# Kernel tuning notes

Hardware: AMD Instinct MI355X
Metric: run time of the kernel (lower is better)

## Reference

```python
import jax, jax.numpy as jnp
import numpy as np

NUM_HEADS = 16
WINDOW = 128


def apply_rope(x):
    # x: (B, H, S, Dh), standard RoPE with half-split rotation, base 10000
    S, Dh = x.shape[-2], x.shape[-1]
    half = Dh // 2
    inv_freq = 1.0 / (10000.0 ** (jnp.arange(half, dtype=jnp.float32) / half))
    ang = jnp.arange(S, dtype=jnp.float32)[:, None] * inv_freq[None, :]  # (S, half)
    cos, sin = jnp.cos(ang), jnp.sin(ang)
    x1, x2 = x[..., :half], x[..., half:]
    return jnp.concatenate([x1 * cos - x2 * sin, x1 * sin + x2 * cos], axis=-1).astype(x.dtype)


def setup_inputs() -> dict:
    key = jax.random.key(0)
    ks = jax.random.split(key, 5)
    D = 1024
    B, S = 2, 2048
    w = 0.02
    return {
        "x": jax.random.normal(ks[0], (B, S, D), dtype=jnp.float32),
        "Wq": jax.random.normal(ks[1], (D, D), dtype=jnp.float32) * w,
        "bq": jnp.zeros((D,), dtype=jnp.float32),
        "Wk": jax.random.normal(ks[2], (D, D), dtype=jnp.float32) * w,
        "bk": jnp.zeros((D,), dtype=jnp.float32),
        "Wv": jax.random.normal(ks[3], (D, D), dtype=jnp.float32) * w,
        "bv": jnp.zeros((D,), dtype=jnp.float32),
        "Wo": jax.random.normal(ks[4], (D, D), dtype=jnp.float32) * w,
        "bo": jnp.zeros((D,), dtype=jnp.float32),
    }


def reference(x, Wq, bq, Wk, bk, Wv, bv, Wo, bo):
    B, S, D = x.shape
    H = NUM_HEADS
    Dh = D // H

    def proj(W, b):
        y = jnp.einsum("bsd,ed->bse", x, W) + b  # nn.Linear: x @ W.T + b
        return y.reshape(B, S, H, Dh).transpose(0, 2, 1, 3)  # (B,H,S,Dh)

    q = apply_rope(proj(Wq, bq)) * (Dh ** -0.5)
    k = apply_rope(proj(Wk, bk))
    v = proj(Wv, bv)

    scores = jnp.einsum("bhqd,bhkd->bhqk", q, k)  # (B,H,S,S)
    idx = jnp.arange(S)
    rel = idx[None, :] - idx[:, None]  # k - q
    blocked = (rel > 0) | (rel < -WINDOW)  # True = masked out
    scores = jnp.where(blocked[None, None], -jnp.inf, scores)
    probs = jax.nn.softmax(scores, axis=-1)
    out = jnp.einsum("bhqk,bhkd->bhqd", probs, v)
    out = out.transpose(0, 2, 1, 3).reshape(B, S, D)
    return jnp.einsum("bsd,ed->bse", out, Wo) + bo
```

## Files before the change

kernel.cpp:

```cpp
#include <hip/hip_runtime.h>

typedef __attribute__((ext_vector_type(8)))  short  short8v;
typedef __attribute__((ext_vector_type(8)))  __bf16 bf16x8;
typedef __attribute__((ext_vector_type(4)))  float  f32x4;

__device__ __forceinline__ short f2bf(float f) {
    unsigned u = __builtin_bit_cast(unsigned, f);
    unsigned r = (u + 0x7fffu + ((u >> 16) & 1u)) >> 16;
    return (short)r;
}
__device__ __forceinline__ float lo16(unsigned u) { return __builtin_bit_cast(float, u << 16); }
__device__ __forceinline__ float hi16(unsigned u) { return __builtin_bit_cast(float, u & 0xffff0000u); }

__device__ __forceinline__ void gload16(const void* g, void* l) {
    __builtin_amdgcn_global_load_lds(
        (const __attribute__((address_space(1))) unsigned*)g,
        (__attribute__((address_space(3))) unsigned*)l, 16, 0, 0);
}

__device__ __forceinline__ void ropePair(const uint4& a, const uint4& b,
                                         const float2* cs8, float scale,
                                         uint4& oa, uint4& ob) {
    const unsigned au[4] = {a.x, a.y, a.z, a.w}, bu[4] = {b.x, b.y, b.z, b.w};
    unsigned ra[4], rb[4];
    #pragma unroll
    for (int wi = 0; wi < 4; ++wi) {
        const float x1l = lo16(au[wi]), x1h = hi16(au[wi]);
        const float x2l = lo16(bu[wi]), x2h = hi16(bu[wi]);
        const float2 cl = cs8[wi * 2], ch = cs8[wi * 2 + 1];
        const float o1l = (x1l * cl.x - x2l * cl.y) * scale;
        const float o2l = (x1l * cl.y + x2l * cl.x) * scale;
        const float o1h = (x1h * ch.x - x2h * ch.y) * scale;
        const float o2h = (x1h * ch.y + x2h * ch.x) * scale;
        ra[wi] = (unsigned)(unsigned short)f2bf(o1l) | ((unsigned)(unsigned short)f2bf(o1h) << 16);
        rb[wi] = (unsigned)(unsigned short)f2bf(o2l) | ((unsigned)(unsigned short)f2bf(o2h) << 16);
    }
    oa = make_uint4(ra[0], ra[1], ra[2], ra[3]);
    ob = make_uint4(rb[0], rb[1], rb[2], rb[3]);
}

#define S_LEN   2048
#define MAT_ELEMS 4194304

__global__ __launch_bounds__(256) void prep(
    const float* __restrict__ x,  const float* __restrict__ Wq,
    const float* __restrict__ Wk, const float* __restrict__ Wv,
    const float* __restrict__ Wo, const float* __restrict__ bq,
    const float* __restrict__ bk, const float* __restrict__ bv,
    short* __restrict__ xb, short* __restrict__ wcat, short* __restrict__ wob,
    float* __restrict__ bcat, float2* __restrict__ tab)
{
    const int tid = blockIdx.x * 256 + threadIdx.x;
    const float4* src;
    short* dst;
    if (tid < 1048576) {
        src = (const float4*)x + tid;  dst = xb + (size_t)tid * 4;
    } else if (tid < 1835008) {
        const int o = tid - 1048576;
        const int mat = o >> 18;
        const int wi  = o & 262143;
        const float* W = (mat == 0) ? Wq : (mat == 1) ? Wk : Wv;
        src = (const float4*)W + wi;  dst = wcat + (size_t)o * 4;
    } else {
        const int o = tid - 1835008;
        src = (const float4*)Wo + o;  dst = wob + (size_t)o * 4;
    }
    const float4 v = *src;
    short4 s4 = make_short4(f2bf(v.x), f2bf(v.y), f2bf(v.z), f2bf(v.w));
    *(short4*)dst = s4;

    if (tid < 65536) {
        const int s  = tid >> 5;
        const int jr = tid & 31;
        const float freq = exp2f(-(float)jr * (13.287712379549449f / 32.0f));
        const float ang  = (float)s * freq;
        tab[tid] = make_float2(cosf(ang), sinf(ang));
    }
    if (tid < 768) {
        const float* B = (tid < 256) ? bq : (tid < 512) ? bk : bv;
        ((float4*)bcat)[tid] = ((const float4*)B)[tid & 255];
    }
}

#define VMC4 do { asm volatile("s_waitcnt vmcnt(4)" ::: "memory"); __builtin_amdgcn_sched_barrier(0); } while (0)
#define VMC0 do { asm volatile("s_waitcnt vmcnt(0)" ::: "memory"); __builtin_amdgcn_sched_barrier(0); } while (0)
#define BAR  __builtin_amdgcn_s_barrier()

#define LOADA(T, PM)                                                      \
  _Pragma("unroll") for (int ii = 0; ii < 4; ++ii) {                      \
    af[ii][0] = ldf(T, fA0, (ii * 32 + (PM) * 128) * 128);                \
    af[ii][1] = ldf(T, fA1, (ii * 32 + (PM) * 128) * 128);                \
  }

#define LOADB(T, PN, BQ)                                                  \
  _Pragma("unroll") for (int jj = 0; jj < 2; ++jj) {                      \
    BQ[jj][0] = ldf(T, fB0, (jj * 64 + (PN) * 128) * 128);                \
    BQ[jj][1] = ldf(T, fB1, (jj * 64 + (PN) * 128) * 128);                \
  }

#define MFMAQ(PM, PN, BQ)                                                     \
  __builtin_amdgcn_s_setprio(1);                                              \
  _Pragma("unroll") for (int ii = 0; ii < 4; ++ii)                            \
    _Pragma("unroll") for (int jj = 0; jj < 2; ++jj) {                        \
      acc[(PM)*4+ii][(PN)*2+jj] = __builtin_amdgcn_mfma_f32_16x16x32_bf16(    \
          af[ii][0], BQ[jj][0], acc[(PM)*4+ii][(PN)*2+jj], 0, 0, 0);          \
      acc[(PM)*4+ii][(PN)*2+jj] = __builtin_amdgcn_mfma_f32_16x16x32_bf16(    \
          af[ii][1], BQ[jj][1], acc[(PM)*4+ii][(PN)*2+jj], 0, 0, 0);          \
    }                                                                         \
  __builtin_amdgcn_s_setprio(0);

#define KTILE(AC, BC, S1, S2, S3, S4, W4)                                 \
  LOADA(AC, 0); LOADB(BC, 0, bq0); S1; BAR; MFMAQ(0, 0, bq0); BAR;        \
  LOADB(BC, 1, bq1); S2; BAR; MFMAQ(0, 1, bq1); BAR;                      \
  LOADA(AC, 1); S3; BAR; MFMAQ(1, 0, bq0); BAR;                           \
  S4; BAR; MFMAQ(1, 1, bq1); W4; BAR;

#define STG(G, KT, H, TILE)                                               \
  { gload16(G + (H) * 262144 + 0     + (KT) * 128, TILE + ((H)*128 + w*16    ) * 64); \
    gload16(G + (H) * 262144 + 16384 + (KT) * 128, TILE + ((H)*128 + w*16 + 8) * 64); }

__global__ __launch_bounds__(512) void gemm8(
    const short* __restrict__ A,
    const short* __restrict__ Bw,
    const float* __restrict__ bias,
    short* __restrict__ outb)
{
    __shared__ short lds[65536];
    short* const Ab0 = lds;
    short* const Bb0 = lds + 16384;
    short* const Ab1 = lds + 32768;
    short* const Bb1 = lds + 49152;

    const int tid = threadIdx.x;
    const int w = tid >> 6, lane = tid & 63;
    const int wm = w >> 2, wn = w & 3;
    const int lr = lane & 15, lg = lane >> 4;

    const int wg  = blockIdx.x;
    const int swz = (wg & 7) * 24 + (wg >> 3);
    const int bx = swz % 12, by = swz / 12;
    const int row0 = by * 256, col0 = bx * 256;

    const int scl  = ((lane & 7) * 16) ^ (((lane >> 3) & 7) << 4);
    const int goff = (w * 16 + (lane >> 3)) * 2048 + scl;
    const char* gA = (const char*)A  + (size_t)row0 * 2048 + goff;
    const char* gB = (const char*)Bw + (size_t)col0 * 2048 + goff;
    const int cswz0 = (lg * 16)      ^ ((lr & 7) << 4);
    const int cswz1 = (64 + lg * 16) ^ ((lr & 7) << 4);
    const int fA0 = (wm * 16 + lr) * 128 + cswz0;
    const int fA1 = (wm * 16 + lr) * 128 + cswz1;
    const int fB0 = (wn * 16 + lr) * 128 + cswz0;
    const int fB1 = (wn * 16 + lr) * 128 + cswz1;

    auto ldf = [&](const short* buf, int voff, int imm) -> bf16x8 {
        return *(const bf16x8*)((const char*)buf + voff + imm);
    };

    f32x4 acc[8][4] = {};
    bf16x8 af[4][2], bq0[2][2], bq1[2][2];

    STG(gA, 0, 0, Ab0);  STG(gB, 0, 0, Bb0);
    STG(gA, 0, 1, Ab0);  STG(gB, 0, 1, Bb0);
    STG(gA, 1, 0, Ab1);  STG(gB, 1, 0, Bb1);
    VMC4;
    BAR;

    #pragma unroll 1
    for (int it = 0; it < 7; ++it) {
        const int t0 = it * 2;
        KTILE(Ab0, Bb0,
              STG(gA, t0 + 1, 1, Ab1),
              STG(gB, t0 + 1, 1, Bb1),
              STG(gA, t0 + 2, 0, Ab0),
              STG(gB, t0 + 2, 0, Bb0), VMC4);
        const int t1 = t0 + 1;
        KTILE(Ab1, Bb1,
              STG(gA, t1 + 1, 1, Ab0),
              STG(gB, t1 + 1, 1, Bb0),
              STG(gA, t1 + 2, 0, Ab1),
              STG(gB, t1 + 2, 0, Bb1), VMC4);
    }
    KTILE(Ab0, Bb0,
          STG(gA, 15, 1, Ab1),
          STG(gB, 15, 1, Bb1), {}, {}, VMC0);
    KTILE(Ab1, Bb1, {}, {}, {}, {}, {});

    const int mat = col0 >> 10;
    const int cm0 = col0 & 1023;
    short* outm = outb + (size_t)mat * MAT_ELEMS;
    #pragma unroll
    for (int j = 0; j < 4; ++j) {
        const int co = wn * 16 + (j & 1) * 64 + (j >> 1) * 128 + lr;
        const float bb = bias[col0 + co];
        #pragma unroll
        for (int i = 0; i < 8; ++i) {
            const int rg = row0 + wm * 16 + (i & 3) * 32 + (i >> 2) * 128 + lg * 4;
            #pragma unroll
            for (int r = 0; r < 4; ++r)
                outm[(size_t)(rg + r) * 1024 + cm0 + co] = f2bf(acc[i][j][r] + bb);
        }
    }
}

__global__ __launch_bounds__(256) void gemm_out(
    const short* __restrict__ A, const short* __restrict__ Bw,
    const float* __restrict__ bias, float* __restrict__ outf)
{
    __shared__ short As[128 * 64];
    __shared__ short Bs[128 * 64];
    const int tid  = threadIdx.x;
    const int w    = tid >> 6, lane = tid & 63;
    const int row0 = blockIdx.y * 128, col0 = blockIdx.x * 128;
    const int wr   = w >> 1, wc = w & 1;
    const int lr   = lane & 15, lg = lane >> 4;
    const int srow = lane >> 3, scol = (lane & 7) * 8;

    f32x4 acc[4][4] = {};

    for (int kt = 0; kt < 16; ++kt) {
        const int k0 = kt * 64;
        __syncthreads();
        #pragma unroll
        for (int rr = 0; rr < 4; ++rr) {
            const int ch = w * 4 + rr;
            const int r  = ch * 8 + srow;
            gload16(A  + (size_t)(row0 + r) * 1024 + k0 + scol, (short*)As + ch * 512);
            gload16(Bw + (size_t)(col0 + r) * 1024 + k0 + scol, (short*)Bs + ch * 512);
        }
        __syncthreads();
        #pragma unroll
        for (int kk = 0; kk < 2; ++kk) {
            const int kb = kk * 32 + lg * 8;
            bf16x8 af[4], bf[4];
            #pragma unroll
            for (int i = 0; i < 4; ++i) {
                af[i] = *(const bf16x8*)&As[(wr * 64 + i * 16 + lr) * 64 + kb];
                bf[i] = *(const bf16x8*)&Bs[(wc * 64 + i * 16 + lr) * 64 + kb];
            }
            #pragma unroll
            for (int i = 0; i < 4; ++i)
                #pragma unroll
                for (int j = 0; j < 4; ++j)
                    acc[i][j] = __builtin_amdgcn_mfma_f32_16x16x32_bf16(af[i], bf[j], acc[i][j], 0, 0, 0);
        }
    }

    #pragma unroll
    for (int i = 0; i < 4; ++i) {
        const int grb = row0 + wr * 64 + i * 16 + lg * 4;
        #pragma unroll
        for (int j = 0; j < 4; ++j) {
            const int cm = col0 + wc * 64 + j * 16 + lr;
            const float bb = bias[cm];
            #pragma unroll
            for (int r = 0; r < 4; ++r)
                outf[(size_t)(grb + r) * 1024 + cm] = acc[i][j][r] + bb;
        }
    }
}

#define KS_ST 72
#define VT_ST 264
#define P_ST  168
__global__ __launch_bounds__(256) void attn_mfma(const short* __restrict__ qkv,
                                                 short* __restrict__ ctx,
                                                 const float2* __restrict__ tab)
{
    __shared__ short lds[27776];
    short* Ks = lds;
    short* VT = lds;
    short* Pl = lds + 16896;
    float* linv = (float*)(lds + 27648);

    const int tid = threadIdx.x;
    const int w = tid >> 6, lane = tid & 63;
    const int g = lane >> 4, l15 = lane & 15;
    const int bid = blockIdx.x;
    const int b  = bid >> 9;
    const int h  = (bid >> 5) & 15;
    const int qb = bid & 31;
    const int qs = qb << 6;
    const size_t rowbase = (size_t)b * S_LEN;
    const int hc = h << 6;

    uint4 vreg[6];
    #pragma unroll
    for (int t = 0; t < 6; ++t) {
        const int c = t * 256 + tid;
        const int key = c >> 3, d0 = c & 7;
        const int gk  = qs - 128 + key;
        const int gkc = gk < 0 ? 0 : gk;
        vreg[t] = *(const uint4*)&qkv[(size_t)2 * MAT_ELEMS + (rowbase + gkc) * 1024 + hc + d0 * 8];
    }

    #pragma unroll
    for (int it = 0; it < 3; ++it) {
        const int c   = it * 256 + tid;
        const int key = c >> 2;
        const int jb  = (c & 3) << 3;
        const int gk  = qs - 128 + key;
        const int gkc = gk < 0 ? 0 : gk;
        const short* kb = qkv + (size_t)1 * MAT_ELEMS + (rowbase + gkc) * 1024 + hc;
        const uint4 k1 = *(const uint4*)(kb + jb);
        const uint4 k2 = *(const uint4*)(kb + jb + 32);
        uint4 o1, o2;
        ropePair(k1, k2, tab + (size_t)gkc * 32 + jb, 1.0f, o1, o2);
        if (gk < 0) { o1 = make_uint4(0, 0, 0, 0); o2 = make_uint4(0, 0, 0, 0); }
        *(uint4*)&Ks[key * KS_ST + jb]      = o1;
        *(uint4*)&Ks[key * KS_ST + jb + 32] = o2;
    }
    __syncthreads();

    const int q = qs + 16 * w + l15;
    const size_t qoff = (rowbase + q) * 1024 + hc;
    const uint4 q1 = *(const uint4*)&qkv[qoff + g * 8];
    const uint4 q2 = *(const uint4*)&qkv[qoff + 32 + g * 8];
    uint4 r1, r2;
    ropePair(q1, q2, tab + (size_t)q * 32 + g * 8, 0.125f, r1, r2);
    const bf16x8 qf0 = __builtin_bit_cast(bf16x8, r1);
    const bf16x8 qf1 = __builtin_bit_cast(bf16x8, r2);

    f32x4 st[9];
    #pragma unroll
    for (int t = 0; t < 9; ++t) {
        const int krow = 16 * w + 16 * t + l15;
        bf16x8 kf0 = *(const bf16x8*)&Ks[krow * KS_ST + g * 8];
        bf16x8 kf1 = *(const bf16x8*)&Ks[krow * KS_ST + 32 + g * 8];
        f32x4 a = {0.f, 0.f, 0.f, 0.f};
        a = __builtin_amdgcn_mfma_f32_16x16x32_bf16(qf0, kf0, a, 0, 0, 0);
        a = __builtin_amdgcn_mfma_f32_16x16x32_bf16(qf1, kf1, a, 0, 0, 0);
        st[t] = a;
    }
    __syncthreads();

    #pragma unroll
    for (int t = 0; t < 6; ++t) {
        const int c = t * 256 + tid;
        const int key = c >> 3, d0 = c & 7;
        const int gk  = qs - 128 + key;
        uint4 vd = vreg[t];
        if (gk < 0) vd = make_uint4(0, 0, 0, 0);
        const unsigned wv[4] = {vd.x, vd.y, vd.z, vd.w};
        #pragma unroll
        for (int e = 0; e < 8; ++e) {
            const short val = (short)(wv[e >> 1] >> (16 * (e & 1)));
            VT[(d0 * 8 + e) * VT_ST + (key ^ (e << 4))] = val;
        }
    }
    {
        const int d  = tid >> 2;
        const int k4 = 12 + (tid & 3);
        const int col0 = (k4 ^ (d & 7)) << 4;
        *(uint4*)&VT[d * VT_ST + col0]     = make_uint4(0, 0, 0, 0);
        *(uint4*)&VT[d * VT_ST + col0 + 8] = make_uint4(0, 0, 0, 0);
    }

    const int jmin = 128 - qs - 16 * w;
    float mrow[4], lsum[4];
    #pragma unroll
    for (int r = 0; r < 4; ++r) mrow[r] = -3.0e38f;
    #pragma unroll
    for (int t = 0; t < 9; ++t) {
        const int jj = 16 * t + l15;
        #pragma unroll
        for (int r = 0; r < 4; ++r) {
            const int qi = 4 * g + r;
            const bool ok = (jj >= qi) && (jj <= qi + 128) && (jj >= jmin);
            if (ok) mrow[r] = fmaxf(mrow[r], st[t][r]);
        }
    }
    #pragma unroll
    for (int r = 0; r < 4; ++r) {
        mrow[r] = fmaxf(mrow[r], __shfl_xor(mrow[r], 1));
        mrow[r] = fmaxf(mrow[r], __shfl_xor(mrow[r], 2));
        mrow[r] = fmaxf(mrow[r], __shfl_xor(mrow[r], 4));
        mrow[r] = fmaxf(mrow[r], __shfl_xor(mrow[r], 8));
        lsum[r] = 0.0f;
    }
    short* Pw = Pl + w * (16 * P_ST);
    #pragma unroll
    for (int t = 0; t < 9; ++t) {
        const int jj = 16 * t + l15;
        #pragma unroll
        for (int r = 0; r < 4; ++r) {
            const int qi = 4 * g + r;
            const bool ok = (jj >= qi) && (jj <= qi + 128) && (jj >= jmin);
            const float p = ok ? __expf(st[t][r] - mrow[r]) : 0.0f;
            lsum[r] += p;
            Pw[qi * P_ST + jj] = f2bf(p);
        }
    }
    {
        short4 z = make_short4(0, 0, 0, 0);
        *(short4*)&Pw[l15 * P_ST + 144 + 4 * g] = z;
    }
    #pragma unroll
    for (int r = 0; r < 4; ++r) {
        lsum[r] += __shfl_xor(lsum[r], 1);
        lsum[r] += __shfl_xor(lsum[r], 2);
        lsum[r] += __shfl_xor(lsum[r], 4);
        lsum[r] += __shfl_xor(lsum[r], 8);
        if (l15 == r) linv[w * 16 + 4 * g + r] = 1.0f / lsum[r];
    }
    __syncthreads();

    f32x4 oc[4] = {};
    #pragma unroll
    for (int kc = 0; kc < 5; ++kc) {
        bf16x8 pf = *(const bf16x8*)&Pw[l15 * P_ST + kc * 32 + g * 8];
        #pragma unroll
        for (int dt = 0; dt < 4; ++dt) {
            const int colb = (16 * w + kc * 32 + g * 8) ^ ((l15 & 7) << 4);
            bf16x8 vf = *(const bf16x8*)&VT[(dt * 16 + l15) * VT_ST + colb];
            oc[dt] = __builtin_amdgcn_mfma_f32_16x16x32_bf16(vf, pf, oc[dt], 0, 0, 0);
        }
    }

    const float inv = linv[w * 16 + l15];
    #pragma unroll
    for (int dt = 0; dt < 4; ++dt) {
        short4 sv;
        sv.x = f2bf(oc[dt][0] * inv);
        sv.y = f2bf(oc[dt][1] * inv);
        sv.z = f2bf(oc[dt][2] * inv);
        sv.w = f2bf(oc[dt][3] * inv);
        *(short4*)&ctx[(rowbase + qs + 16 * w + l15) * 1024 + hc + dt * 16 + 4 * g] = sv;
    }
}

extern "C" void kernel_launch(void* const* d_in, const int* in_sizes, int n_in,
                              void* d_out, int out_size, void* d_ws, size_t ws_size,
                              hipStream_t stream) {
    const float* x  = (const float*)d_in[0];
    const float* Wq = (const float*)d_in[1];
    const float* bq = (const float*)d_in[2];
    const float* Wk = (const float*)d_in[3];
    const float* bk = (const float*)d_in[4];
    const float* Wv = (const float*)d_in[5];
    const float* bv = (const float*)d_in[6];
    const float* Wo = (const float*)d_in[7];
    const float* bo = (const float*)d_in[8];

    char* ws = (char*)d_ws;
    short*  xb   = (short*) (ws + 0);
    short*  wcat = (short*) (ws + 8388608);
    short*  wob  = (short*) (ws + 14680064);
    short*  qkv  = (short*) (ws + 16777216);
    short*  ctx  = (short*) (ws + 41943040);
    float2* tab  = (float2*)(ws + 50331648);
    float*  bcat = (float*) (ws + 50855936);

    prep<<<8192, 256, 0, stream>>>(x, Wq, Wk, Wv, Wo, bq, bk, bv,
                                   xb, wcat, wob, bcat, tab);
    gemm8<<<192, 512, 0, stream>>>(xb, wcat, bcat, qkv);
    attn_mfma<<<1024, 256, 0, stream>>>(qkv, ctx, tab);
    gemm_out<<<dim3(8, 32), 256, 0, stream>>>(ctx, wob, bo, (float*)d_out);
}
```

Before: 95.70 us.

## Restructure GEMM pipeline with double-buffered register fragments and full-tile prefetch

Reworks the QKV GEMM main loop so that A and B register fragments are double-buffered. The next tile's first fragments are loaded from LDS during the current tile's last MFMA quarters, and whole next k-tiles are staged into LDS with a vmcnt(8) wait instead of vmcnt(4). The aim is to hide LDS read latency and global load latency behind MFMA work. Separately, the attention kernel's V-transpose LDS stride is padded from 264 to 266 to reduce bank conflicts, which slightly grows the shared memory footprint. The deeper prefetch raises register and vmcnt pressure and makes the waits harder to get right.

Result: slower. 101.9 us (+6.5%).

```diff
diff --git a/kernel.cpp b/kernel.cpp
--- a/kernel.cpp
+++ b/kernel.cpp
@@ -82,42 +82,44 @@
     }
 }
 
+#define VMC8 do { asm volatile("s_waitcnt vmcnt(8)" ::: "memory"); __builtin_amdgcn_sched_barrier(0); } while (0)
 #define VMC4 do { asm volatile("s_waitcnt vmcnt(4)" ::: "memory"); __builtin_amdgcn_sched_barrier(0); } while (0)
 #define VMC0 do { asm volatile("s_waitcnt vmcnt(0)" ::: "memory"); __builtin_amdgcn_sched_barrier(0); } while (0)
 #define BAR  __builtin_amdgcn_s_barrier()
 
-#define LOADA(T, PM)                                                      \
-  _Pragma("unroll") for (int ii = 0; ii < 4; ++ii) {                      \
-    af[ii][0] = ldf(T, fA0, (ii * 32 + (PM) * 128) * 128);                \
-    af[ii][1] = ldf(T, fA1, (ii * 32 + (PM) * 128) * 128);                \
-  }
-
-#define LOADB(T, PN, BQ)                                                  \
-  _Pragma("unroll") for (int jj = 0; jj < 2; ++jj) {                      \
-    BQ[jj][0] = ldf(T, fB0, (jj * 64 + (PN) * 128) * 128);                \
-    BQ[jj][1] = ldf(T, fB1, (jj * 64 + (PN) * 128) * 128);                \
-  }
-
-#define MFMAQ(PM, PN, BQ)                                                     \
+#define LD_A0(T) _Pragma("unroll") for (int ii = 0; ii < 4; ++ii) { \
+    aA[ii][0] = ldf(T, fA0, (ii * 32) * 128);                        \
+    aA[ii][1] = ldf(T, fA1, (ii * 32) * 128); }
+#define LD_A1(T) _Pragma("unroll") for (int ii = 0; ii < 4; ++ii) { \
+    aB[ii][0] = ldf(T, fA0, (ii * 32 + 128) * 128);                  \
+    aB[ii][1] = ldf(T, fA1, (ii * 32 + 128) * 128); }
+#define LD_B0(T) _Pragma("unroll") for (int jj = 0; jj < 2; ++jj) { \
+    bA[jj][0] = ldf(T, fB0, (jj * 64) * 128);                        \
+    bA[jj][1] = ldf(T, fB1, (jj * 64) * 128); }
+#define LD_B1(T) _Pragma("unroll") for (int jj = 0; jj < 2; ++jj) { \
+    bB[jj][0] = ldf(T, fB0, (jj * 64 + 128) * 128);                  \
+    bB[jj][1] = ldf(T, fB1, (jj * 64 + 128) * 128); }
+
+#define MFQ(PM, PN, AF, BF)                                                   \
   __builtin_amdgcn_s_setprio(1);                                              \
   _Pragma("unroll") for (int ii = 0; ii < 4; ++ii)                            \
     _Pragma("unroll") for (int jj = 0; jj < 2; ++jj) {                        \
       acc[(PM)*4+ii][(PN)*2+jj] = __builtin_amdgcn_mfma_f32_16x16x32_bf16(    \
-          af[ii][0], BQ[jj][0], acc[(PM)*4+ii][(PN)*2+jj], 0, 0, 0);          \
+          AF[ii][0], BF[jj][0], acc[(PM)*4+ii][(PN)*2+jj], 0, 0, 0);          \
       acc[(PM)*4+ii][(PN)*2+jj] = __builtin_amdgcn_mfma_f32_16x16x32_bf16(    \
-          af[ii][1], BQ[jj][1], acc[(PM)*4+ii][(PN)*2+jj], 0, 0, 0);          \
+          AF[ii][1], BF[jj][1], acc[(PM)*4+ii][(PN)*2+jj], 0, 0, 0);          \
     }                                                                         \
   __builtin_amdgcn_s_setprio(0);
 
-#define KTILE(AC, BC, S1, S2, S3, S4, W4)                                 \
-  LOADA(AC, 0); LOADB(BC, 0, bq0); S1; BAR; MFMAQ(0, 0, bq0); BAR;        \
-  LOADB(BC, 1, bq1); S2; BAR; MFMAQ(0, 1, bq1); BAR;                      \
-  LOADA(AC, 1); S3; BAR; MFMAQ(1, 0, bq0); BAR;                           \
-  S4; BAR; MFMAQ(1, 1, bq1); W4; BAR;
-
-#define STG(G, KT, H, TILE)                                               \
-  { gload16(G + (H) * 262144 + 0     + (KT) * 128, TILE + ((H)*128 + w*16    ) * 64); \
-    gload16(G + (H) * 262144 + 16384 + (KT) * 128, TILE + ((H)*128 + w*16 + 8) * 64); }
+#define KT(AC, BC, AN, BN, S1, S2, S3, S4, V1, V2, V3, V4)  \
+  LD_B1(BC); S1; V1; BAR; MFQ(0, 0, aA, bA); BAR;           \
+  LD_A1(AC); S2; V2; BAR; MFQ(0, 1, aA, bB); BAR;           \
+  LD_A0(AN); S3; V3; BAR; MFQ(1, 0, aB, bA); BAR;           \
+  LD_B0(BN); S4; V4; BAR; MFQ(1, 1, aB, bB); BAR;
+
+#define STG(G, KT_, H, TILE)                                               \
+  { gload16(G + (H) * 262144 + 0     + (KT_) * 128, TILE + ((H)*128 + w*16    ) * 64); \
+    gload16(G + (H) * 262144 + 16384 + (KT_) * 128, TILE + ((H)*128 + w*16 + 8) * 64); }
 
 __global__ __launch_bounds__(512) void gemm8(
     const short* __restrict__ A,
@@ -157,33 +159,31 @@
     };
 
     f32x4 acc[8][4] = {};
-    bf16x8 af[4][2], bq0[2][2], bq1[2][2];
-
-    STG(gA, 0, 0, Ab0);  STG(gB, 0, 0, Bb0);
-    STG(gA, 0, 1, Ab0);  STG(gB, 0, 1, Bb0);
-    STG(gA, 1, 0, Ab1);  STG(gB, 1, 0, Bb1);
-    VMC4;
+    bf16x8 aA[4][2], aB[4][2], bA[2][2], bB[2][2];
+
+    STG(gA, 0, 0, Ab0); STG(gB, 0, 0, Bb0); STG(gB, 0, 1, Bb0); STG(gA, 0, 1, Ab0);
+    STG(gA, 1, 0, Ab1); STG(gB, 1, 0, Bb1); STG(gB, 1, 1, Bb1); STG(gA, 1, 1, Ab1);
+    VMC8;
     BAR;
+    LD_A0(Ab0); LD_B0(Bb0);
 
     #pragma unroll 1
     for (int it = 0; it < 7; ++it) {
         const int t0 = it * 2;
-        KTILE(Ab0, Bb0,
-              STG(gA, t0 + 1, 1, Ab1),
-              STG(gB, t0 + 1, 1, Bb1),
-              STG(gA, t0 + 2, 0, Ab0),
-              STG(gB, t0 + 2, 0, Bb0), VMC4);
-        const int t1 = t0 + 1;
-        KTILE(Ab1, Bb1,
-              STG(gA, t1 + 1, 1, Ab0),
-              STG(gB, t1 + 1, 1, Bb0),
-              STG(gA, t1 + 2, 0, Ab1),
-              STG(gB, t1 + 2, 0, Bb1), VMC4);
-    }
-    KTILE(Ab0, Bb0,
-          STG(gA, 15, 1, Ab1),
-          STG(gB, 15, 1, Bb1), {}, {}, VMC0);
-    KTILE(Ab1, Bb1, {}, {}, {}, {}, {});
+        KT(Ab0, Bb0, Ab1, Bb1,
+           STG(gA, t0 + 2, 0, Ab0), STG(gB, t0 + 2, 0, Bb0),
+           STG(gB, t0 + 2, 1, Bb0), STG(gA, t0 + 2, 1, Ab0),
+           VMC8, VMC8, VMC8, VMC8)
+        KT(Ab1, Bb1, Ab0, Bb0,
+           STG(gA, t0 + 3, 0, Ab1), STG(gB, t0 + 3, 0, Bb1),
+           STG(gB, t0 + 3, 1, Bb1), STG(gA, t0 + 3, 1, Ab1),
+           VMC8, VMC8, VMC8, VMC8)
+    }
+    KT(Ab0, Bb0, Ab1, Bb1, {}, {}, {}, {}, VMC4, {}, VMC0, {})
+    LD_B1(Bb1); BAR; MFQ(0, 0, aA, bA); BAR;
+    LD_A1(Ab1); BAR; MFQ(0, 1, aA, bB); BAR;
+    BAR; MFQ(1, 0, aB, bA); BAR;
+    BAR; MFQ(1, 1, aB, bB); BAR;
 
     const int mat = col0 >> 10;
     const int cm0 = col0 & 1023;
@@ -260,17 +260,17 @@
 }
 
 #define KS_ST 72
-#define VT_ST 264
+#define VT_ST 266
 #define P_ST  168
 __global__ __launch_bounds__(256) void attn_mfma(const short* __restrict__ qkv,
                                                  short* __restrict__ ctx,
                                                  const float2* __restrict__ tab)
 {
-    __shared__ short lds[27776];
+    __shared__ short lds[27904];
     short* Ks = lds;
     short* VT = lds;
-    short* Pl = lds + 16896;
-    float* linv = (float*)(lds + 27648);
+    short* Pl = lds + 17024;
+    float* linv = (float*)(lds + 27776);
 
     const int tid = threadIdx.x;
     const int w = tid >> 6, lane = tid & 63;
```
